# Optimization experiments

Measured on AMD Instinct MI355X. Metric: run time of the kernel, lower is better.

Reference implementation:

```python
import jax, jax.numpy as jnp
import numpy as np

N, D = 16384, 128
T = 0.07  # temperature


def setup_inputs() -> dict:
    key = jax.random.key(0)
    x = jax.random.normal(key, (N, D), dtype=jnp.float32)
    # uniformity loss assumes unit-norm embeddings (else exp(||x||^2 / t) overflows)
    x = x / jnp.linalg.norm(x, axis=-1, keepdims=True)
    return {"x": x}


def reference(x):
    # x.matmul(x.T).div(t).exp().sum(-1).log().mean()
    sims = jnp.matmul(x, x.T) / T            # [N, N]
    return jnp.mean(jnp.log(jnp.sum(jnp.exp(sims), axis=-1)))
```

## Files before the change

kernel.cpp:

```cpp
#include <hip/hip_runtime.h>
#include <hip/hip_bf16.h>

#define NN 16384
#define DD 128
#define TS 64
#define NS 256
#define NTILES 32896
#define NB 1024
#define SQRT_SCALE 4.5398159622f

#define EXP_A 8388608.0f
#define EXP_K 1064986316.0f

typedef __attribute__((ext_vector_type(8))) short bf16x8;
typedef __attribute__((ext_vector_type(4))) float f32x4;

#define TRI(s) (256 * (s) - ((s) * ((s)-1)) / 2)

__global__ void convert_swz(const float* __restrict__ x, ushort* __restrict__ xb) {
    int t = blockIdx.x * blockDim.x + threadIdx.x;
    int r = t >> 4;
    int c = t & 15;
    const float4* src = (const float4*)(x + (size_t)r * DD + c * 8);
    float4 f0 = src[0];
    float4 f1 = src[1];
    float vals[8] = {f0.x, f0.y, f0.z, f0.w, f1.x, f1.y, f1.z, f1.w};
    bf16x8 v;
#pragma unroll
    for (int i = 0; i < 8; ++i) {
        __hip_bfloat16 h = __float2bfloat16(vals[i] * SQRT_SCALE);
        v[i] = (short)__builtin_bit_cast(unsigned short, h);
    }
    int cs = c ^ (r & 15);
    *(bf16x8*)(xb + (size_t)r * DD + cs * 8) = v;
}

__global__ __launch_bounds__(256, 4) void gemm_exp_tri(const ushort* __restrict__ xb,
                                                       float* __restrict__ rowsum) {
    __shared__ __align__(16) char lds[4][2][4096];

    const int tid  = threadIdx.x;
    const int lane = tid & 63;
    const int cw   = tid >> 6;
    const int frow = lane & 15;
    const int kq   = lane >> 4;

    char* myL = &lds[cw][0][0];

    const int bid = blockIdx.x;
    const int R0 = (int)(((long long)bid * NTILES) >> 10);
    const int R1 = (int)(((long long)(bid + 1) * NTILES) >> 10);
    const int n  = R1 - R0;

    int s = (int)(256.5f - sqrtf(256.5f * 256.5f - 2.0f * (float)R0));
    if (s < 0) s = 0;
    if (s > 255) s = 255;
    while (s < 255 && TRI(s + 1) <= R0) ++s;
    while (s > 0 && TRI(s) > R0) --s;
    int ct = s + (R0 - TRI(s));

    auto stage = [&](int buf, int c) {
        const char* g = (const char*)(xb + (size_t)(c * TS + cw * 16) * DD);
#pragma unroll
        for (int j = 0; j < 4; ++j) {
            __builtin_amdgcn_global_load_lds(
                (const __attribute__((address_space(1))) unsigned int*)(g + j * 1024 + lane * 16),
                (__attribute__((address_space(3))) unsigned int*)(myL + buf * 4096 + j * 1024),
                16, 0, 0);
        }
    };

    int ps = s, pc = ct;
    stage(0, pc);
    if (pc == 255) { ++ps; pc = ps; } else ++pc;
    stage(1, pc);
    if (pc == 255) { ++ps; pc = ps; } else ++pc;

    bf16x8 af[4][4];
    auto load_af = [&](int ss) {
#pragma unroll
        for (int m = 0; m < 4; ++m)
#pragma unroll
            for (int kk = 0; kk < 4; ++kk) {
                int ra = ss * TS + m * 16 + frow;
                int slot = (kk * 4 + kq) ^ frow;
                af[m][kk] = *(const bf16x8*)(xb + (size_t)ra * DD + slot * 8);
            }
    };
    load_af(s);

    int roff[4];
#pragma unroll
    for (int kk = 0; kk < 4; ++kk)
        roff[kk] = frow * 256 + ((((kk << 2) + kq) ^ frow) << 4);

    asm volatile("s_waitcnt vmcnt(0)" ::: "memory");

    const f32x4 zacc = {0.f, 0.f, 0.f, 0.f};
    float rs[4][4] = {};

    auto flush_rows = [&](int ss) {
#pragma unroll
        for (int m = 0; m < 4; ++m)
#pragma unroll
            for (int j = 0; j < 4; ++j) {
                float v = rs[m][j];
                v += __shfl_xor(v, 1);
                v += __shfl_xor(v, 2);
                v += __shfl_xor(v, 4);
                v += __shfl_xor(v, 8);
                rs[m][j] = v;
            }
        if (frow == 0) {
#pragma unroll
            for (int m = 0; m < 4; ++m)
#pragma unroll
                for (int j = 0; j < 4; ++j)
                    atomicAdd(&rowsum[ss * TS + m * 16 + kq * 4 + j], rs[m][j]);
        }
    };

    for (int q = 0; q < n; ++q) {
        const int cur = q & 1;
        const char* Bb = myL + cur * 4096;

        f32x4 acc[4];
        __builtin_amdgcn_s_setprio(1);
#pragma unroll
        for (int kk = 0; kk < 4; ++kk) {
            bf16x8 bfr = *(const bf16x8*)(Bb + roff[kk]);
            if (kk == 0) {
#pragma unroll
                for (int m = 0; m < 4; ++m)
                    acc[m] = __builtin_amdgcn_mfma_f32_16x16x32_bf16(
                        af[m][0], bfr, zacc, 0, 0, 0);
            } else {
#pragma unroll
                for (int m = 0; m < 4; ++m)
                    acc[m] = __builtin_amdgcn_mfma_f32_16x16x32_bf16(
                        af[m][kk], bfr, acc[m], 0, 0, 0);
            }
        }
        __builtin_amdgcn_s_setprio(0);

        __builtin_amdgcn_sched_barrier(0);
        if (q + 2 < n) {
            stage(cur, pc);
            if (pc == 255) { ++ps; pc = ps; } else ++pc;
        }

        float cs = 0.f;
#pragma unroll
        for (int m = 0; m < 4; ++m)
#pragma unroll
            for (int j = 0; j < 4; ++j) {
                float b = __builtin_fmaf(acc[m][j], EXP_A, EXP_K);
                float e = __builtin_bit_cast(float, (int)b);
                rs[m][j] += e;
                cs += e;
            }
        cs += __shfl_xor(cs, 16);
        cs += __shfl_xor(cs, 32);
        if (ct != s && kq == 0)
            atomicAdd(&rowsum[ct * TS + cw * 16 + frow], cs);

        if (q + 1 < n) {
            int olds = s;
            if (ct == 255) { ++s; ct = s; } else ++ct;
            if (s != olds) {
                flush_rows(olds);
#pragma unroll
                for (int m = 0; m < 4; ++m)
#pragma unroll
                    for (int j = 0; j < 4; ++j)
                        rs[m][j] = 0.f;
                load_af(s);
                asm volatile("s_waitcnt vmcnt(0)" ::: "memory");
            } else if (q < n - 2) {
                asm volatile("s_waitcnt vmcnt(4)" ::: "memory");
            } else {
                asm volatile("s_waitcnt vmcnt(0)" ::: "memory");
            }
        }
    }

    flush_rows(s);
}

__global__ void finalize_part(const float* __restrict__ rowsum,
                              float* __restrict__ partial) {
    const int tid = threadIdx.x;
    const int r = blockIdx.x * 256 + tid;
    float s = __builtin_amdgcn_logf(rowsum[r]) * 0.69314718056f;
#pragma unroll
    for (int o = 1; o < 64; o <<= 1)
        s += __shfl_xor(s, o);
    __shared__ float wsum[4];
    if ((tid & 63) == 0) wsum[tid >> 6] = s;
    __syncthreads();
    if (tid == 0)
        partial[blockIdx.x] = wsum[0] + wsum[1] + wsum[2] + wsum[3];
}

__global__ void finalize_sum(const float* __restrict__ partial, float* __restrict__ out) {
    float s = partial[threadIdx.x];
#pragma unroll
    for (int o = 1; o < 64; o <<= 1)
        s += __shfl_xor(s, o);
    if (threadIdx.x == 0)
        out[0] = s * (1.0f / NN);
}

extern "C" void kernel_launch(void* const* d_in, const int* in_sizes, int n_in,
                              void* d_out, int out_size, void* d_ws, size_t ws_size,
                              hipStream_t stream) {
    const float* x = (const float*)d_in[0];
    float* out = (float*)d_out;

    ushort* xb     = (ushort*)d_ws;
    float* rowsum  = (float*)((char*)d_ws + (size_t)NN * DD * 2);
    float* partial = rowsum + NN;

    hipMemsetAsync(rowsum, 0, NN * sizeof(float), stream);
    convert_swz<<<(NN * 16) / 256, 256, 0, stream>>>(x, xb);
    gemm_exp_tri<<<NB, 256, 0, stream>>>(xb, rowsum);
    finalize_part<<<64, 256, 0, stream>>>(rowsum, partial);
    finalize_sum<<<1, 64, 0, stream>>>(partial, out);
}
```

Measured before the change: 86.77 us.

## Replace per-tile column atomics with bf16 scratch writes plus column reduction kernel

Instead of issuing a float atomicAdd per column of each off-diagonal tile into rowsum, the GEMM kernel writes each tile's column sums as bf16 into a scratch buffer indexed by tile rank. A new colreduce kernel then sums each column block's contributions across tiles and adds them to rowsum. This removes contended global atomics from the hot loop, at the cost of an extra kernel launch, scratch traffic, and reduced precision on the partial column sums. The vmcnt wait is bumped to account for the extra store.

```diff
diff --git a/kernel.cpp b/kernel.cpp
--- a/kernel.cpp
+++ b/kernel.cpp
@@ -36,7 +36,8 @@
 }
 
 __global__ __launch_bounds__(256, 4) void gemm_exp_tri(const ushort* __restrict__ xb,
-                                                       float* __restrict__ rowsum) {
+                                                       float* __restrict__ rowsum,
+                                                       ushort* __restrict__ colscr) {
     __shared__ __align__(16) char lds[4][2][4096];
 
     const int tid  = threadIdx.x;
@@ -161,8 +162,11 @@
             }
         cs += __shfl_xor(cs, 16);
         cs += __shfl_xor(cs, 32);
-        if (ct != s && kq == 0)
-            atomicAdd(&rowsum[ct * TS + cw * 16 + frow], cs);
+        if (kq == 0) {
+            ushort v = (ct == s) ? (ushort)0
+                     : __builtin_bit_cast(ushort, __float2bfloat16(cs));
+            colscr[(size_t)(R0 + q) * TS + cw * 16 + frow] = v;
+        }
 
         if (q + 1 < n) {
             int olds = s;
@@ -177,7 +181,7 @@
                 load_af(s);
                 asm volatile("s_waitcnt vmcnt(0)" ::: "memory");
             } else if (q < n - 2) {
-                asm volatile("s_waitcnt vmcnt(4)" ::: "memory");
+                asm volatile("s_waitcnt vmcnt(5)" ::: "memory");
             } else {
                 asm volatile("s_waitcnt vmcnt(0)" ::: "memory");
             }
@@ -185,6 +189,33 @@
     }
 
     flush_rows(s);
+}
+
+__global__ __launch_bounds__(512) void colreduce(const ushort* __restrict__ colscr,
+                                                 float* __restrict__ rowsum) {
+    const int ct  = blockIdx.x;
+    const int tid = threadIdx.x;
+    const int i   = tid & 63;
+    const int p   = tid >> 6;
+
+    float acc = 0.f;
+#pragma unroll 4
+    for (int s = p; s <= ct; s += 8) {
+        int rank = TRI(s) + (ct - s);
+        ushort u = colscr[(size_t)rank * TS + i];
+        __hip_bfloat16 h = __builtin_bit_cast(__hip_bfloat16, u);
+        acc += __bfloat162float(h);
+    }
+
+    __shared__ float part[8][64];
+    part[p][i] = acc;
+    __syncthreads();
+    if (p == 0) {
+        float t = 0.f;
+#pragma unroll
+        for (int q = 0; q < 8; ++q) t += part[q][i];
+        rowsum[ct * TS + i] += t;
+    }
 }
 
 __global__ void finalize_part(const float* __restrict__ rowsum,
@@ -217,13 +248,15 @@
     const float* x = (const float*)d_in[0];
     float* out = (float*)d_out;
 
-    ushort* xb     = (ushort*)d_ws;
-    float* rowsum  = (float*)((char*)d_ws + (size_t)NN * DD * 2);
-    float* partial = rowsum + NN;
+    ushort* xb      = (ushort*)d_ws;
+    float* rowsum   = (float*)((char*)d_ws + (size_t)NN * DD * 2);
+    float* partial  = rowsum + NN;
+    ushort* colscr  = (ushort*)(partial + 64);
 
     hipMemsetAsync(rowsum, 0, NN * sizeof(float), stream);
     convert_swz<<<(NN * 16) / 256, 256, 0, stream>>>(x, xb);
-    gemm_exp_tri<<<NB, 256, 0, stream>>>(xb, rowsum);
+    gemm_exp_tri<<<NB, 256, 0, stream>>>(xb, rowsum, colscr);
+    colreduce<<<NS, 512, 0, stream>>>(colscr, rowsum);
     finalize_part<<<64, 256, 0, stream>>>(rowsum, partial);
     finalize_sum<<<1, 64, 0, stream>>>(partial, out);
 }
```

Measured after the change: 94.82 us. +9.3%, slower.

## Replace LDS staging with register B loads and defer column sums to reduce kernel

Applied to the files above, without the earlier changes.

Drops the global_load_lds double buffer and loads B fragments straight into registers, ping-ponging between two register sets across an unrolled two-iteration loop. Per-tile column sums are no longer added with atomics; they are written as bf16 values to a scratch buffer and summed by a new colreduce kernel. The block count is doubled and the occupancy hint lowered. This removes LDS traffic and atomic contention, but adds scratch writes, an extra launch, bf16 rounding of partial sums, and loses the explicit waitcnt control.

```diff
diff --git a/kernel.cpp b/kernel.cpp
--- a/kernel.cpp
+++ b/kernel.cpp
@@ -6,7 +6,7 @@
 #define TS 64
 #define NS 256
 #define NTILES 32896
-#define NB 1024
+#define NB 2048
 #define SQRT_SCALE 4.5398159622f
 
 #define EXP_A 8388608.0f
@@ -35,21 +35,18 @@
     *(bf16x8*)(xb + (size_t)r * DD + cs * 8) = v;
 }
 
-__global__ __launch_bounds__(256, 4) void gemm_exp_tri(const ushort* __restrict__ xb,
-                                                       float* __restrict__ rowsum) {
-    __shared__ __align__(16) char lds[4][2][4096];
-
+__global__ __launch_bounds__(256, 3) void gemm_exp_tri(const ushort* __restrict__ xb,
+                                                       float* __restrict__ rowsum,
+                                                       ushort* __restrict__ colscr) {
     const int tid  = threadIdx.x;
     const int lane = tid & 63;
     const int cw   = tid >> 6;
     const int frow = lane & 15;
     const int kq   = lane >> 4;
 
-    char* myL = &lds[cw][0][0];
-
     const int bid = blockIdx.x;
-    const int R0 = (int)(((long long)bid * NTILES) >> 10);
-    const int R1 = (int)(((long long)(bid + 1) * NTILES) >> 10);
+    const int R0 = (int)(((long long)bid * NTILES) >> 11);
+    const int R1 = (int)(((long long)(bid + 1) * NTILES) >> 11);
     const int n  = R1 - R0;
 
     int s = (int)(256.5f - sqrtf(256.5f * 256.5f - 2.0f * (float)R0));
@@ -59,42 +56,38 @@
     while (s > 0 && TRI(s) > R0) --s;
     int ct = s + (R0 - TRI(s));
 
-    auto stage = [&](int buf, int c) {
-        const char* g = (const char*)(xb + (size_t)(c * TS + cw * 16) * DD);
-#pragma unroll
-        for (int j = 0; j < 4; ++j) {
-            __builtin_amdgcn_global_load_lds(
-                (const __attribute__((address_space(1))) unsigned int*)(g + j * 1024 + lane * 16),
-                (__attribute__((address_space(3))) unsigned int*)(myL + buf * 4096 + j * 1024),
-                16, 0, 0);
-        }
+    int slot[4];
+#pragma unroll
+    for (int kk = 0; kk < 4; ++kk)
+        slot[kk] = ((((kk << 2) | kq) ^ frow) << 3);
+
+    const ushort* bbase = xb + (size_t)(cw * 16 + frow) * DD;
+
+    auto bload = [&](bf16x8 (&buf)[4], int c) {
+        const ushort* p = bbase + (size_t)c * (TS * DD);
+#pragma unroll
+        for (int kk = 0; kk < 4; ++kk)
+            buf[kk] = *(const bf16x8*)(p + slot[kk]);
     };
 
     int ps = s, pc = ct;
-    stage(0, pc);
-    if (pc == 255) { ++ps; pc = ps; } else ++pc;
-    stage(1, pc);
-    if (pc == 255) { ++ps; pc = ps; } else ++pc;
+    auto adv = [&]() { if (pc == 255) { ++ps; pc = ps; } else ++pc; };
+
+    bf16x8 bA[4], bB[4];
+    bload(bA, pc); adv();
+    bload(bB, pc); adv();
 
     bf16x8 af[4][4];
     auto load_af = [&](int ss) {
 #pragma unroll
-        for (int m = 0; m < 4; ++m)
-#pragma unroll
-            for (int kk = 0; kk < 4; ++kk) {
-                int ra = ss * TS + m * 16 + frow;
-                int slot = (kk * 4 + kq) ^ frow;
-                af[m][kk] = *(const bf16x8*)(xb + (size_t)ra * DD + slot * 8);
-            }
+        for (int m = 0; m < 4; ++m) {
+            const ushort* p = xb + (size_t)(ss * TS + m * 16 + frow) * DD;
+#pragma unroll
+            for (int kk = 0; kk < 4; ++kk)
+                af[m][kk] = *(const bf16x8*)(p + slot[kk]);
+        }
     };
     load_af(s);
-
-    int roff[4];
-#pragma unroll
-    for (int kk = 0; kk < 4; ++kk)
-        roff[kk] = frow * 256 + ((((kk << 2) + kq) ^ frow) << 4);
-
-    asm volatile("s_waitcnt vmcnt(0)" ::: "memory");
 
     const f32x4 zacc = {0.f, 0.f, 0.f, 0.f};
     float rs[4][4] = {};
@@ -120,34 +113,26 @@
         }
     };
 
-    for (int q = 0; q < n; ++q) {
-        const int cur = q & 1;
-        const char* Bb = myL + cur * 4096;
-
+    auto body = [&](bf16x8 (&buf)[4], int q) {
         f32x4 acc[4];
         __builtin_amdgcn_s_setprio(1);
 #pragma unroll
         for (int kk = 0; kk < 4; ++kk) {
-            bf16x8 bfr = *(const bf16x8*)(Bb + roff[kk]);
             if (kk == 0) {
 #pragma unroll
                 for (int m = 0; m < 4; ++m)
                     acc[m] = __builtin_amdgcn_mfma_f32_16x16x32_bf16(
-                        af[m][0], bfr, zacc, 0, 0, 0);
+                        af[m][0], buf[0], zacc, 0, 0, 0);
             } else {
 #pragma unroll
                 for (int m = 0; m < 4; ++m)
                     acc[m] = __builtin_amdgcn_mfma_f32_16x16x32_bf16(
-                        af[m][kk], bfr, acc[m], 0, 0, 0);
+                        af[m][kk], buf[kk], acc[m], 0, 0, 0);
             }
         }
         __builtin_amdgcn_s_setprio(0);
 
-        __builtin_amdgcn_sched_barrier(0);
-        if (q + 2 < n) {
-            stage(cur, pc);
-            if (pc == 255) { ++ps; pc = ps; } else ++pc;
-        }
+        if (q + 2 < n) { bload(buf, pc); adv(); }
 
         float cs = 0.f;
 #pragma unroll
@@ -159,10 +144,9 @@
                 rs[m][j] += e;
                 cs += e;
             }
-        cs += __shfl_xor(cs, 16);
-        cs += __shfl_xor(cs, 32);
-        if (ct != s && kq == 0)
-            atomicAdd(&rowsum[ct * TS + cw * 16 + frow], cs);
+        ushort v = (ct == s) ? (ushort)0
+                 : __builtin_bit_cast(ushort, __float2bfloat16(cs));
+        colscr[(size_t)(R0 + q) * 256 + (cw << 6) + lane] = v;
 
         if (q + 1 < n) {
             int olds = s;
@@ -175,16 +159,50 @@
                     for (int j = 0; j < 4; ++j)
                         rs[m][j] = 0.f;
                 load_af(s);
-                asm volatile("s_waitcnt vmcnt(0)" ::: "memory");
-            } else if (q < n - 2) {
-                asm volatile("s_waitcnt vmcnt(4)" ::: "memory");
-            } else {
-                asm volatile("s_waitcnt vmcnt(0)" ::: "memory");
-            }
-        }
+            }
+        }
+    };
+
+    for (int q = 0; q < n; q += 2) {
+        body(bA, q);
+        if (q + 1 < n) body(bB, q + 1);
     }
 
     flush_rows(s);
+}
+
+__global__ __launch_bounds__(256) void colreduce(const ushort* __restrict__ colscr,
+                                                 float* __restrict__ rowsum) {
+    const int k = blockIdx.x;
+    const int p = k >> 1;
+    const int h = k & 1;
+    const int e = threadIdx.x;
+
+    const int ctA = p, ctB = 255 - p;
+    float aA = 0.f, aB = 0.f;
+#pragma unroll 4
+    for (int s = h; s <= ctA; s += 2) {
+        int rank = TRI(s) + (ctA - s);
+        aA += __bfloat162float(__builtin_bit_cast(__hip_bfloat16,
+                  colscr[(size_t)rank * 256 + e]));
+    }
+#pragma unroll 4
+    for (int s = h; s <= ctB; s += 2) {
+        int rank = TRI(s) + (ctB - s);
+        aB += __bfloat162float(__builtin_bit_cast(__hip_bfloat16,
+                  colscr[(size_t)rank * 256 + e]));
+    }
+
+    __shared__ float pA[256], pB[256];
+    pA[e] = aA; pB[e] = aB;
+    __syncthreads();
+    if (e < 64) {
+        int base = (e >> 4) * 64 + (e & 15);
+        float vA = pA[base] + pA[base + 16] + pA[base + 32] + pA[base + 48];
+        float vB = pB[base] + pB[base + 16] + pB[base + 32] + pB[base + 48];
+        atomicAdd(&rowsum[ctA * TS + e], vA);
+        atomicAdd(&rowsum[ctB * TS + e], vB);
+    }
 }
 
 __global__ void finalize_part(const float* __restrict__ rowsum,
@@ -217,13 +235,15 @@
     const float* x = (const float*)d_in[0];
     float* out = (float*)d_out;
 
-    ushort* xb     = (ushort*)d_ws;
-    float* rowsum  = (float*)((char*)d_ws + (size_t)NN * DD * 2);
-    float* partial = rowsum + NN;
+    ushort* xb      = (ushort*)d_ws;
+    float* rowsum   = (float*)((char*)d_ws + (size_t)NN * DD * 2);
+    float* partial  = rowsum + NN;
+    ushort* colscr  = (ushort*)(partial + 64);
 
     hipMemsetAsync(rowsum, 0, NN * sizeof(float), stream);
     convert_swz<<<(NN * 16) / 256, 256, 0, stream>>>(x, xb);
-    gemm_exp_tri<<<NB, 256, 0, stream>>>(xb, rowsum);
+    gemm_exp_tri<<<NB, 256, 0, stream>>>(xb, rowsum, colscr);
+    colreduce<<<256, 256, 0, stream>>>(colscr, rowsum);
     finalize_part<<<64, 256, 0, stream>>>(rowsum, partial);
     finalize_sum<<<1, 64, 0, stream>>>(partial, out);
 }
```

New measurement: 92.93 us. 7.1% more time.
